# Performance work log

Measured on AMD Instinct MI355X. Metric: run time of the kernel, lower is better.

## Reference

```python
import jax, jax.numpy as jnp
import numpy as np

DELAY = 5
EMBED = 64


def setup_inputs() -> dict:
    key = jax.random.key(0)
    kx, k1, k2 = jax.random.split(key, 3)
    B, S, E = 2, 512, EMBED
    L = DELAY * E                      # linear terms = 320
    F = 1 + L + L * (L + 1) // 2       # 51681 total polynomial features
    x = jax.random.normal(kx, (B, S, E), dtype=jnp.float32)
    # readout: Linear(F->E) -> GELU -> Linear(E->E); weights stored [in, out]
    W1 = jax.random.normal(k1, (F, E), dtype=jnp.float32) * (1.0 / np.sqrt(F))
    b1 = jnp.zeros((E,), dtype=jnp.float32)
    W2 = jax.random.normal(k2, (E, E), dtype=jnp.float32) * (1.0 / np.sqrt(E))
    b2 = jnp.zeros((E,), dtype=jnp.float32)
    return {"x": x, "W1": W1, "b1": b1, "W2": W2, "b2": b2}


def reference(x, W1, b1, W2, b2):
    B, S, E = x.shape
    L = DELAY * E
    # causal delay window: pad delay-1 zeros at sequence start
    xp = jnp.pad(x, ((0, 0), (DELAY - 1, 0), (0, 0)))
    # torch unfold(1, delay, 1) -> [B, S, E, delay]; flatten index = e*delay + k
    delayed = jnp.stack([xp[:, k:k + S, :] for k in range(DELAY)], axis=-1)
    feats = delayed.reshape(B, S, L)  # linear terms
    # quadratic terms: all pairs i<=j in flattened order (upper triangle incl. diag)
    iu, ju = np.triu_indices(L)
    quad = feats[..., iu] * feats[..., ju]          # [B, S, L*(L+1)//2]
    const = jnp.ones((B, S, 1), dtype=feats.dtype)
    allf = jnp.concatenate([const, feats, quad], axis=-1)  # [B, S, F]
    h = jax.nn.gelu(allf @ W1 + b1, approximate=False)     # exact GELU like torch
    return h @ W2 + b2
```

## Files before the change

### kernel.cpp

```cpp
#include <hip/hip_runtime.h>
#include <hip/hip_bf16.h>
#include <math.h>


#define NF     51681
#define KPAD   352
#define KCHK   11
#define NFR    24
#define NPAD   (NFR * 16)
#define MT2    128
#define ATS    768
#define XWS    133

typedef __attribute__((ext_vector_type(8))) short short8;
typedef __attribute__((ext_vector_type(4))) float f32x4;

#define W1C_BYTES  ((size_t)64 * NF * 2)
#define MF_BYTES   ((size_t)64 * KPAD * NPAD * 2)
#define HBUF_OFF   (W1C_BYTES + MF_BYTES)

__device__ __forceinline__ unsigned short f2bf(float x) {
    return __bfloat16_as_ushort(__float2bfloat16(x));
}
__device__ __forceinline__ float bf2f(unsigned short h) {
    union { unsigned u; float f; } v; v.u = ((unsigned)h) << 16; return v.f;
}

__global__ void k_t(const float* __restrict__ W1, unsigned short* __restrict__ W1c) {
    __shared__ float t[64 * 65];
    const int tid = threadIdx.x;
    const int f0 = blockIdx.x * 64;
    #pragma unroll 1
    for (int r = 0; r < 16; ++r) {
        int idx = r * 256 + tid;
        int fi = idx >> 6, e = idx & 63;
        t[fi * 65 + e] = (f0 + fi < NF) ? W1[(size_t)(f0 + fi) * 64 + e] : 0.f;
    }
    __syncthreads();
    #pragma unroll 1
    for (int r = 0; r < 16; ++r) {
        int idx = r * 256 + tid;
        int e = idx >> 6, fi = idx & 63;
        if (f0 + fi < NF)
            W1c[(size_t)e * NF + f0 + fi] = f2bf(t[fi * 65 + e]);
    }
}

__global__ void k_pack(const unsigned short* __restrict__ W1c,
                       unsigned short* __restrict__ Mfrag) {
    const int g = blockIdx.x * 256 + threadIdx.x;
    const int lane = g & 63;
    const int rec = g >> 6;
    const int nf = rec % NFR;
    const int rec2 = rec / NFR;
    const int kc = rec2 % KCHK;
    const int e = rec2 / KCHK;
    const int i = nf * 16 + (lane & 15);
    const int jb = kc * 32 + ((lane >> 4) << 3);
    const unsigned short* wrow = W1c + (size_t)e * NF;

    __attribute__((aligned(16))) unsigned short v[8];
    #pragma unroll
    for (int r = 0; r < 8; ++r) {
        int j = jb + r;
        unsigned short out = 0;
        if (i <= j && j <= 320) {
            if (j == 320) {
                out = (i == 320) ? wrow[0] : wrow[1 + i];
            } else {
                int idx = 321 + i * 320 - ((i * (i - 1)) >> 1) + (j - i);
                out = wrow[idx];
            }
        }
        v[r] = out;
    }
    *(short8*)(Mfrag + (size_t)g * 8) = *(short8*)v;
}

__global__ __launch_bounds__(1024, 1) void k_main(const float* __restrict__ x,
                                                  const unsigned short* __restrict__ Mfrag,
                                                  float* __restrict__ hbuf) {
    __shared__ unsigned short At[MT2 * (ATS / 2)];
    __shared__ float xw[64 * XWS];
    __shared__ float hpart[2][8][64];

    const int tid = threadIdx.x;
    const int bid = blockIdx.x;
    const int tile = bid >> 5;
    const int ep = bid & 31;
    const int e0 = ep * 2;
    const int tok0 = tile * MT2;
    const int b = tile >> 2, s0 = (tile & 3) * MT2;

    #pragma unroll 1
    for (int idx = tid; idx < 132 * 64; idx += 1024) {
        int r = idx >> 6, ee = idx & 63;
        int s = s0 - 4 + r;
        xw[ee * XWS + r] = (s >= 0) ? x[((b << 9) + s) * 64 + ee] : 0.f;
    }
    __syncthreads();

    char* Atb = (char*)At;
    #pragma unroll 1
    for (int rec = tid; rec < MT2 * 48; rec += 1024) {
        int t = rec / 48, jr = rec - t * 48;
        int j0 = jr * 8;
        __attribute__((aligned(16))) unsigned short hv[8];
        #pragma unroll
        for (int r = 0; r < 8; ++r) {
            int j = j0 + r;
            float v;
            if (j < 320) { int e5 = j / 5, k = j - e5 * 5; v = xw[e5 * XWS + t + k]; }
            else v = (j == 320) ? 1.0f : 0.f;
            hv[r] = f2bf(v);
        }
        *(short8*)(Atb + t * ATS + ((j0 * 2) ^ ((t & 7) << 4))) = *(short8*)hv;
    }
    __syncthreads();

    const int lane = tid & 63, wv = tid >> 6;
    const int wm = wv >> 3, wn = wv & 7;
    const int nf0 = wn * 3;
    const int arow = wm * 64 + (lane & 15);
    const int aslot = (lane >> 4) << 4;

    int ibase[3]; float isel1[3], isel0[3];
    #pragma unroll
    for (int q = 0; q < 3; ++q) {
        int i = (nf0 + q) * 16 + (lane & 15);
        int ic = (i < 320) ? i : 0;
        ibase[q] = (ic / 5) * XWS + (ic % 5);
        isel1[q] = (i < 320) ? 1.f : 0.f;
        isel0[q] = (i == 320) ? 1.f : 0.f;
    }

    #pragma unroll 1
    for (int eo = 0; eo < 2; ++eo) {
        const unsigned short* Bbase = Mfrag + (size_t)(e0 + eo) * (KPAD * NPAD);

        f32x4 acc[4][3];
        #pragma unroll
        for (int mf = 0; mf < 4; ++mf)
            #pragma unroll
            for (int q = 0; q < 3; ++q) acc[mf][q] = f32x4{0.f,0.f,0.f,0.f};

        short8 B0[3], B1[3];

#define BLD(DST, KCV)                                                              \
    do { if ((KCV) < KCHK) {                                                       \
        _Pragma("unroll")                                                          \
        for (int q = 0; q < 3; ++q)                                                \
            DST[q] = *(const short8*)(Bbase +                                      \
                ((size_t)(((KCV) * NFR + nf0 + q) * 64 + lane)) * 8);              \
    } } while (0)

#define STEP(KCV, CUR)                                                             \
    do {                                                                           \
        short8 Af[4];                                                              \
        _Pragma("unroll")                                                          \
        for (int mf = 0; mf < 4; ++mf) {                                           \
            int t = arow + mf * 16;                                                \
            int jb = (KCV) * 64 + aslot;                                           \
            Af[mf] = *(const short8*)(Atb + t * ATS + (jb ^ ((t & 7) << 4)));      \
        }                                                                          \
        __builtin_amdgcn_s_setprio(1);                                             \
        _Pragma("unroll")                                                          \
        for (int mf = 0; mf < 4; ++mf) {                                           \
            _Pragma("unroll")                                                      \
            for (int q = 0; q < 3; ++q)                                            \
                acc[mf][q] = __builtin_amdgcn_mfma_f32_16x16x32_bf16(              \
                    Af[mf], CUR[q], acc[mf][q], 0, 0, 0);                          \
        }                                                                          \
        __builtin_amdgcn_s_setprio(0);                                             \
    } while (0)

        BLD(B0, 0);
        BLD(B1, 1);
        #pragma unroll 1
        for (int kc = 0; kc < KCHK - 1; kc += 2) {
            STEP(kc, B0);
            BLD(B0, kc + 2);
            STEP(kc + 1, B1);
            BLD(B1, kc + 3);
        }
        STEP(KCHK - 1, B0);
#undef STEP
#undef BLD

        float s[4][4];
        #pragma unroll
        for (int mf = 0; mf < 4; ++mf)
            #pragma unroll
            for (int r = 0; r < 4; ++r) s[mf][r] = 0.f;

        #pragma unroll
        for (int q = 0; q < 3; ++q) {
            #pragma unroll
            for (int mf = 0; mf < 4; ++mf)
                #pragma unroll
                for (int r = 0; r < 4; ++r) {
                    int t = wm * 64 + mf * 16 + ((lane >> 4) << 2) + r;
                    float dv = isel1[q] * xw[ibase[q] + t] + isel0[q];
                    s[mf][r] += acc[mf][q][r] * dv;
                }
        }
        #pragma unroll
        for (int mf = 0; mf < 4; ++mf)
            #pragma unroll
            for (int r = 0; r < 4; ++r) {
                float v = s[mf][r];
                v += __shfl_xor(v, 1);
                v += __shfl_xor(v, 2);
                v += __shfl_xor(v, 4);
                v += __shfl_xor(v, 8);
                s[mf][r] = v;
            }
        if ((lane & 15) == 0) {
            #pragma unroll
            for (int mf = 0; mf < 4; ++mf)
                #pragma unroll
                for (int r = 0; r < 4; ++r)
                    hpart[wm][wn][mf * 16 + ((lane >> 4) << 2) + r] = s[mf][r];
        }
        __syncthreads();
        if (tid < 128) {
            int wmx = tid >> 6, tl = tid & 63;
            float v = 0.f;
            #pragma unroll
            for (int w = 0; w < 8; ++w) v += hpart[wmx][w][tl];
            hbuf[(size_t)(tok0 + wmx * 64 + tl) * 64 + (e0 + eo)] = v;
        }
        __syncthreads();
    }
}

__global__ void k_epi(const float* __restrict__ hbuf, const float* __restrict__ b1,
                      const float* __restrict__ W2, const float* __restrict__ b2,
                      float* __restrict__ out) {
    __shared__ float h[4 * 64];
    int tid = threadIdx.x;
    int t = tid >> 6, e = tid & 63;
    int token = blockIdx.x * 4 + t;
    float pre = hbuf[token * 64 + e] + b1[e];
    float hv = 0.5f * pre * (1.0f + erff(pre * 0.70710678118654752f));
    h[t * 64 + e] = hv;
    __syncthreads();
    float s = b2[e];
    #pragma unroll 8
    for (int ee = 0; ee < 64; ++ee)
        s += h[t * 64 + ee] * W2[ee * 64 + e];
    out[token * 64 + e] = s;
}

extern "C" void kernel_launch(void* const* d_in, const int* in_sizes, int n_in,
                              void* d_out, int out_size, void* d_ws, size_t ws_size,
                              hipStream_t stream) {
    const float* x  = (const float*)d_in[0];
    const float* W1 = (const float*)d_in[1];
    const float* b1 = (const float*)d_in[2];
    const float* W2 = (const float*)d_in[3];
    const float* b2 = (const float*)d_in[4];
    float* out = (float*)d_out;

    unsigned short* W1c   = (unsigned short*)d_ws;
    unsigned short* Mfrag = (unsigned short*)((char*)d_ws + W1C_BYTES);
    float* hbuf           = (float*)((char*)d_ws + HBUF_OFF);

    k_t<<<(NF + 63) / 64, 256, 0, stream>>>(W1, W1c);
    k_pack<<<4224, 256, 0, stream>>>(W1c, Mfrag);
    k_main<<<256, 1024, 0, stream>>>(x, Mfrag, hbuf);
    k_epi<<<256, 256, 0, stream>>>(hbuf, b1, W2, b2, out);
}
```

Baseline: 54.63 us.

## Skip zero upper-triangle K chunks and precompute A tiles in a prep kernel

The main GEMM now starts each wave's K loop at a chunk offset derived from its N-fragment group. This skips K chunks that are entirely zero because the quadratic weight matrix is upper triangular, and k_pack likewise skips writing those chunks. Building the delayed-feature A tile and the diagonal multiplier values moves into a new k_aprep kernel that writes bf16 images to workspace. k_main then just copies the image into LDS and reads the multipliers from global memory. Waves are remapped so light and heavy K workloads are paired within a SIMD, at the cost of an extra launch, extra global traffic, and bf16 rounding of the multiplier.

Result: slower. 75.83 us (+38.8%).

```diff
diff --git a/kernel.cpp b/kernel.cpp
--- a/kernel.cpp
+++ b/kernel.cpp
@@ -10,7 +10,6 @@
 #define NPAD   (NFR * 16)
 #define MT2    128
 #define ATS    768
-#define XWS    133
 
 typedef __attribute__((ext_vector_type(8))) short short8;
 typedef __attribute__((ext_vector_type(4))) float f32x4;
@@ -18,6 +17,10 @@
 #define W1C_BYTES  ((size_t)64 * NF * 2)
 #define MF_BYTES   ((size_t)64 * KPAD * NPAD * 2)
 #define HBUF_OFF   (W1C_BYTES + MF_BYTES)
+#define AIMG_OFF   (HBUF_OFF + (size_t)1024 * 64 * 4)
+#define AIMG_SH_PER_TILE 49152
+#define DC_OFF     (AIMG_OFF + (size_t)8 * AIMG_SH_PER_TILE * 2)
+#define DC_SH_PER_TILE 49152
 
 __device__ __forceinline__ unsigned short f2bf(float x) {
     return __bfloat16_as_ushort(__float2bfloat16(x));
@@ -55,6 +58,10 @@
     const int rec2 = rec / NFR;
     const int kc = rec2 % KCHK;
     const int e = rec2 / KCHK;
+
+    const int kc0o = (3 * (nf / 3)) >> 1;
+    if (kc < kc0o) return;
+
     const int i = nf * 16 + (lane & 15);
     const int jb = kc * 32 + ((lane >> 4) << 3);
     const unsigned short* wrow = W1c + (size_t)e * NF;
@@ -77,11 +84,61 @@
     *(short8*)(Mfrag + (size_t)g * 8) = *(short8*)v;
 }
 
-__global__ __launch_bounds__(1024, 1) void k_main(const float* __restrict__ x,
+__global__ void k_aprep(const float* __restrict__ x, unsigned short* __restrict__ Aimg,
+                        unsigned short* __restrict__ DC) {
+    __shared__ float xwin[132 * 65];
+    const int tile = blockIdx.x >> 2;
+    const int qtr  = blockIdx.x & 3;
+    const int tid = threadIdx.x;
+    const int b = tile >> 2, s0 = (tile & 3) * 128;
+
+    #pragma unroll 1
+    for (int idx = tid; idx < 132 * 64; idx += 256) {
+        int r = idx >> 6, ee = idx & 63;
+        int s = s0 - 4 + r;
+        xwin[r * 65 + ee] = (s >= 0) ? x[((b << 9) + s) * 64 + ee] : 0.f;
+    }
+    __syncthreads();
+
+    unsigned short* ai = Aimg + (size_t)tile * AIMG_SH_PER_TILE;
+    #pragma unroll 1
+    for (int rec = qtr * 1536 + tid; rec < (qtr + 1) * 1536; rec += 256) {
+        int t = rec / 48;
+        int s16 = (rec - t * 48) * 16;
+        int j0 = (s16 ^ ((t & 7) << 4)) >> 1;
+        __attribute__((aligned(16))) unsigned short hv[8];
+        #pragma unroll
+        for (int r = 0; r < 8; ++r) {
+            int j = j0 + r;
+            float v;
+            if (j < 320) { int e5 = j / 5, k = j - e5 * 5; v = xwin[(t + k) * 65 + e5]; }
+            else v = (j == 320) ? 1.0f : 0.f;
+            hv[r] = f2bf(v);
+        }
+        *(short8*)(ai + t * 384 + (s16 >> 1)) = *(short8*)hv;
+    }
+
+    unsigned short* dc = DC + (size_t)tile * DC_SH_PER_TILE;
+    #pragma unroll 1
+    for (int g = qtr * 12288 + tid; g < (qtr + 1) * 12288; g += 256) {
+        int lane = g & 63, rec = g >> 6;
+        int r = rec & 3;
+        int nf = (rec >> 2) % NFR;
+        int mfw = rec / 96;
+        int t = mfw * 16 + ((lane >> 4) << 2) + r;
+        int i = nf * 16 + (lane & 15);
+        float v;
+        if (i < 320) { int e5 = i / 5, k = i - e5 * 5; v = xwin[(t + k) * 65 + e5]; }
+        else v = (i == 320) ? 1.0f : 0.f;
+        dc[g] = f2bf(v);
+    }
+}
+
+__global__ __launch_bounds__(1024, 1) void k_main(const unsigned short* __restrict__ Aimg,
                                                   const unsigned short* __restrict__ Mfrag,
+                                                  const unsigned short* __restrict__ DC,
                                                   float* __restrict__ hbuf) {
     __shared__ unsigned short At[MT2 * (ATS / 2)];
-    __shared__ float xw[64 * XWS];
     __shared__ float hpart[2][8][64];
 
     const int tid = threadIdx.x;
@@ -90,49 +147,25 @@
     const int ep = bid & 31;
     const int e0 = ep * 2;
     const int tok0 = tile * MT2;
-    const int b = tile >> 2, s0 = (tile & 3) * MT2;
-
-    #pragma unroll 1
-    for (int idx = tid; idx < 132 * 64; idx += 1024) {
-        int r = idx >> 6, ee = idx & 63;
-        int s = s0 - 4 + r;
-        xw[ee * XWS + r] = (s >= 0) ? x[((b << 9) + s) * 64 + ee] : 0.f;
+
+    {
+        const short8* src = (const short8*)(Aimg + (size_t)tile * AIMG_SH_PER_TILE);
+        short8* dst = (short8*)At;
+        #pragma unroll
+        for (int k = 0; k < 6; ++k)
+            dst[k * 1024 + tid] = src[k * 1024 + tid];
     }
     __syncthreads();
 
-    char* Atb = (char*)At;
-    #pragma unroll 1
-    for (int rec = tid; rec < MT2 * 48; rec += 1024) {
-        int t = rec / 48, jr = rec - t * 48;
-        int j0 = jr * 8;
-        __attribute__((aligned(16))) unsigned short hv[8];
-        #pragma unroll
-        for (int r = 0; r < 8; ++r) {
-            int j = j0 + r;
-            float v;
-            if (j < 320) { int e5 = j / 5, k = j - e5 * 5; v = xw[e5 * XWS + t + k]; }
-            else v = (j == 320) ? 1.0f : 0.f;
-            hv[r] = f2bf(v);
-        }
-        *(short8*)(Atb + t * ATS + ((j0 * 2) ^ ((t & 7) << 4))) = *(short8*)hv;
-    }
-    __syncthreads();
-
     const int lane = tid & 63, wv = tid >> 6;
-    const int wm = wv >> 3, wn = wv & 7;
+    const int wm = wv >> 3;
+    const int w3 = wv & 3;
+    const int wn = (wv & 4) ? (7 - w3) : w3;
     const int nf0 = wn * 3;
+    const int kc0 = (3 * wn) >> 1;
     const int arow = wm * 64 + (lane & 15);
     const int aslot = (lane >> 4) << 4;
-
-    int ibase[3]; float isel1[3], isel0[3];
-    #pragma unroll
-    for (int q = 0; q < 3; ++q) {
-        int i = (nf0 + q) * 16 + (lane & 15);
-        int ic = (i < 320) ? i : 0;
-        ibase[q] = (ic / 5) * XWS + (ic % 5);
-        isel1[q] = (i < 320) ? 1.f : 0.f;
-        isel0[q] = (i == 320) ? 1.f : 0.f;
-    }
+    char* Atb = (char*)At;
 
     #pragma unroll 1
     for (int eo = 0; eo < 2; ++eo) {
@@ -174,16 +207,17 @@
         __builtin_amdgcn_s_setprio(0);                                             \
     } while (0)
 
-        BLD(B0, 0);
-        BLD(B1, 1);
+        BLD(B0, kc0);
+        BLD(B1, kc0 + 1);
+        int kc = kc0;
         #pragma unroll 1
-        for (int kc = 0; kc < KCHK - 1; kc += 2) {
+        for (; kc + 1 < KCHK; kc += 2) {
             STEP(kc, B0);
             BLD(B0, kc + 2);
             STEP(kc + 1, B1);
             BLD(B1, kc + 3);
         }
-        STEP(KCHK - 1, B0);
+        if (kc < KCHK) STEP(kc, B0);
 #undef STEP
 #undef BLD
 
@@ -193,15 +227,16 @@
             #pragma unroll
             for (int r = 0; r < 4; ++r) s[mf][r] = 0.f;
 
+        const unsigned short* DCb = DC + (size_t)tile * DC_SH_PER_TILE + lane;
         #pragma unroll
         for (int q = 0; q < 3; ++q) {
             #pragma unroll
             for (int mf = 0; mf < 4; ++mf)
                 #pragma unroll
                 for (int r = 0; r < 4; ++r) {
-                    int t = wm * 64 + mf * 16 + ((lane >> 4) << 2) + r;
-                    float dv = isel1[q] * xw[ibase[q] + t] + isel0[q];
-                    s[mf][r] += acc[mf][q][r] * dv;
+                    unsigned short dv =
+                        DCb[((wm * 4 + mf) * 96 + (nf0 + q) * 4 + r) * 64];
+                    s[mf][r] += acc[mf][q][r] * bf2f(dv);
                 }
         }
         #pragma unroll
@@ -265,9 +300,12 @@
     unsigned short* W1c   = (unsigned short*)d_ws;
     unsigned short* Mfrag = (unsigned short*)((char*)d_ws + W1C_BYTES);
     float* hbuf           = (float*)((char*)d_ws + HBUF_OFF);
+    unsigned short* Aimg  = (unsigned short*)((char*)d_ws + AIMG_OFF);
+    unsigned short* DC    = (unsigned short*)((char*)d_ws + DC_OFF);
 
     k_t<<<(NF + 63) / 64, 256, 0, stream>>>(W1, W1c);
     k_pack<<<4224, 256, 0, stream>>>(W1c, Mfrag);
-    k_main<<<256, 1024, 0, stream>>>(x, Mfrag, hbuf);
+    k_aprep<<<32, 256, 0, stream>>>(x, Aimg, DC);
+    k_main<<<256, 1024, 0, stream>>>(Aimg, Mfrag, DC, hbuf);
     k_epi<<<256, 256, 0, stream>>>(hbuf, b1, W2, b2, out);
 }
```
